# Optimization experiments

Hardware: AMD Instinct MI355X
Metric: run time of the kernel (lower is better)

## Reference

```python
import jax, jax.numpy as jnp
import numpy as np

N_NODES = 32768
N_EDGES = 524288
IN_F = 256
OUT_F = 128
NB = 4


def setup_inputs() -> dict:
    key = jax.random.key(0)
    ks = jax.random.split(key, 12)
    s_in = 1.0 / np.sqrt(IN_F)
    s_out = 1.0 / np.sqrt(OUT_F)
    s_cat = 1.0 / np.sqrt(OUT_F * NB)
    return {
        "x": jax.random.normal(ks[0], (N_NODES, IN_F), dtype=jnp.float32),
        "edge_index": jax.random.randint(ks[1], (2, N_EDGES), 0, N_NODES, dtype=jnp.int64),
        "Wb": jax.random.uniform(ks[2], (NB, IN_F, OUT_F), jnp.float32, -s_in, s_in),
        "bb": jax.random.uniform(ks[3], (NB, OUT_F), jnp.float32, -s_in, s_in),
        "W1": jax.random.uniform(ks[4], (NB, OUT_F, OUT_F), jnp.float32, -s_out, s_out),
        "b1": jax.random.uniform(ks[5], (NB, OUT_F), jnp.float32, -s_out, s_out),
        "W2": jax.random.uniform(ks[6], (NB, OUT_F, OUT_F), jnp.float32, -s_out, s_out),
        "b2": jax.random.uniform(ks[7], (NB, OUT_F), jnp.float32, -s_out, s_out),
        "branch_gates": jnp.ones((NB,), dtype=jnp.float32),
        "temperature": jnp.asarray(1.0, dtype=jnp.float32),
        "Wo": jax.random.uniform(ks[8], (OUT_F * NB, OUT_F), jnp.float32, -s_cat, s_cat),
        "bo": jax.random.uniform(ks[9], (OUT_F,), jnp.float32, -s_cat, s_cat),
    }


def _scatter_mean_step(h, row, col, inv_deg):
    # gather per-edge source features, mean-reduce onto destination nodes
    sums = jax.ops.segment_sum(h[row], col, num_segments=N_NODES)
    return sums * inv_deg


def reference(x, edge_index, Wb, bb, W1, b1, W2, b2, branch_gates, temperature, Wo, bo):
    row, col = edge_index[0], edge_index[1]
    deg = jax.ops.segment_sum(jnp.ones((N_EDGES,), x.dtype), col, num_segments=N_NODES)
    inv_deg = (1.0 / jnp.maximum(deg, 1.0))[:, None]  # empty segments -> 0 (scatter_mean semantics)

    gates = jax.nn.softmax(branch_gates / temperature)

    branch_outputs = []
    for i in range(NB):
        h = x @ Wb[i] + bb[i]                   # [N, OUT_F]
        for _ in range(i):                       # scale = scales[i % 4] = i
            h = _scatter_mean_step(h, row, col, inv_deg)
        h = jax.nn.relu(h @ W1[i] + b1[i]) @ W2[i] + b2[i]
        branch_outputs.append(h * gates[i])

    concat = jnp.concatenate(branch_outputs, axis=1)  # [N, NB*OUT_F]
    return concat @ Wo + bo
```

## Files before the change

### kernel.cpp

```cpp
#include <hip/hip_runtime.h>
#include <math.h>

#define N_NODES 32768
#define N_EDGES 524288
#define IN_F    256
#define OUT_F   128
#define NB      4
#define STRIDE  96

#define NE_BLK   256
#define CONV_BLK 1024
#define GX_BLK   2048
#define GEMM_BLK (N_NODES / 128)
#define M_BLK    (N_NODES / 256)

typedef __attribute__((ext_vector_type(8))) short bf16x8;
typedef __attribute__((ext_vector_type(4))) float f32x4;
typedef __attribute__((ext_vector_type(4))) ushort u16x4;

__device__ __forceinline__ ushort f2b(float f) {
    uint u = __float_as_uint(f);
    return (ushort)((u + 0x7fffu + ((u >> 16) & 1u)) >> 16);
}
__device__ __forceinline__ float b2f_lo(uint v) { return __uint_as_float(v << 16); }
__device__ __forceinline__ float b2f_hi(uint v) { return __uint_as_float(v & 0xffff0000u); }

__device__ __forceinline__ float softmax_gate(const float* bg, const float* temp, int i) {
    float T = temp[0];
    float mx = fmaxf(fmaxf(bg[0], bg[1]), fmaxf(bg[2], bg[3]));
    float e0 = expf((bg[0] - mx) / T), e1 = expf((bg[1] - mx) / T);
    float e2 = expf((bg[2] - mx) / T), e3 = expf((bg[3] - mx) / T);
    float s = e0 + e1 + e2 + e3;
    float ei = (i == 0) ? e0 : (i == 1) ? e1 : (i == 2) ? e2 : e3;
    return ei / s;
}

__device__ __forceinline__ int detect_i32(const int* __restrict__ ei, int* sflag) {
    if (threadIdx.x < 64) {
        unsigned long long b = __ballot(ei[2 * threadIdx.x + 1] != 0);
        if (threadIdx.x == 0) *sflag = (b != 0ull) ? 1 : 0;
    }
    __syncthreads();
    return *sflag;
}

__global__ __launch_bounds__(256) void fill_all_kernel(
    const int* __restrict__ ei, int* __restrict__ cursor, int* __restrict__ srcs,
    const float* __restrict__ x, ushort* __restrict__ xb,
    const float* __restrict__ Wb, const float* __restrict__ W1,
    const float* __restrict__ W2, const float* __restrict__ Wo,
    const float* __restrict__ bb, const float* __restrict__ b2,
    const float* __restrict__ bo, const float* __restrict__ bg,
    const float* __restrict__ temp,
    ushort* __restrict__ WcT, ushort* __restrict__ WzT,
    float* __restrict__ u, float* __restrict__ cvec) {
    __shared__ float smem[16 * 128];
    __shared__ int sflag;
    int b = blockIdx.x;
    int tid = threadIdx.x;
    if (b < NE_BLK) {
        int i32 = detect_i32(ei, &sflag);
#pragma unroll
        for (int it = 0; it < 8; it++) {
            int e = b * 2048 + it * 256 + tid;
            int r, c;
            if (i32 == 0) {
                r = __builtin_nontemporal_load(ei + 2 * e);
                c = __builtin_nontemporal_load(ei + 2 * (N_EDGES + e));
            } else {
                r = __builtin_nontemporal_load(ei + e);
                c = __builtin_nontemporal_load(ei + N_EDGES + e);
            }
            int slot = atomicAdd(&cursor[c], 1);
            if (slot < STRIDE) srcs[(size_t)c * STRIDE + slot] = r;
        }
        return;
    }
    b -= NE_BLK;
    if (b < CONV_BLK) {
#pragma unroll
        for (int it = 0; it < 8; it++) {
            int idx = b * 2048 + it * 256 + tid;
            f32x4 v = __builtin_nontemporal_load((const f32x4*)x + idx);
            u16x4 o;
            o.x = f2b(v.x); o.y = f2b(v.y); o.z = f2b(v.z); o.w = f2b(v.w);
            *((u16x4*)xb + idx) = o;
        }
        return;
    }
    b -= CONV_BLK;
    int f = tid & 127, rh = tid >> 7;
    if (b < 64) {
        int i = b >> 4, k0 = (b & 15) * 16;
#pragma unroll
        for (int rr = 0; rr < 8; rr++)
            smem[(rh * 8 + rr) * 128 + f] = Wb[((size_t)i * IN_F + k0 + rh * 8 + rr) * OUT_F + f];
        __syncthreads();
        float acc[8] = {};
        const float* W1i = W1 + (size_t)i * OUT_F * OUT_F;
        for (int j = 0; j < OUT_F; j++) {
            float w1 = W1i[j * OUT_F + f];
#pragma unroll
            for (int rr = 0; rr < 8; rr++) acc[rr] += smem[(rh * 8 + rr) * 128 + j] * w1;
        }
        ushort tmp[8];
#pragma unroll
        for (int rr = 0; rr < 8; rr++) tmp[rr] = f2b(acc[rr]);
        *(uint4*)(WcT + ((size_t)i * OUT_F + f) * IN_F + k0 + rh * 8) = *(uint4*)tmp;
    } else if (b < 96) {
        int id = b - 64;
        int i = id >> 3, j0 = (id & 7) * 16;
#pragma unroll
        for (int rr = 0; rr < 8; rr++)
            smem[(rh * 8 + rr) * 128 + f] = W2[((size_t)i * OUT_F + j0 + rh * 8 + rr) * OUT_F + f];
        __syncthreads();
        float acc[8] = {};
        for (int l = 0; l < OUT_F; l++) {
            float wo = Wo[((size_t)i * OUT_F + l) * OUT_F + f];
#pragma unroll
            for (int rr = 0; rr < 8; rr++) acc[rr] += smem[(rh * 8 + rr) * 128 + l] * wo;
        }
        float g = softmax_gate(bg, temp, i);
        ushort tmp[8];
#pragma unroll
        for (int rr = 0; rr < 8; rr++) tmp[rr] = f2b(g * acc[rr]);
        *(uint4*)(WzT + (size_t)f * (NB * OUT_F) + i * OUT_F + j0 + rh * 8) = *(uint4*)tmp;
    } else {
        int id = b - 96;
        int jc = rh;
        if (id < NB) {
            int i = id;
            float partial = 0.f;
            for (int j = jc * 64; j < jc * 64 + 64; j++)
                partial += bb[i * OUT_F + j] * W1[((size_t)i * OUT_F + j) * OUT_F + f];
            smem[jc * 128 + f] = partial;
            __syncthreads();
            if (jc == 0) u[i * OUT_F + f] = smem[f] + smem[128 + f];
        } else {
            int i = id - NB;
            float partial = 0.f;
            for (int j = jc * 64; j < jc * 64 + 64; j++)
                partial += b2[i * OUT_F + j] * Wo[((size_t)i * OUT_F + j) * OUT_F + f];
            smem[jc * 128 + f] = partial;
            __syncthreads();
            if (jc == 0) {
                float tot = (smem[f] + smem[128 + f]) * softmax_gate(bg, temp, i);
                if (i == 0) tot += bo[f];
                atomicAdd(&cvec[f], tot);
            }
        }
    }
}

#define ACC8(A, V)                                                              \
    A[0] += b2f_lo(V.x); A[1] += b2f_hi(V.x);                                   \
    A[2] += b2f_lo(V.y); A[3] += b2f_hi(V.y);                                   \
    A[4] += b2f_lo(V.z); A[5] += b2f_hi(V.z);                                   \
    A[6] += b2f_lo(V.w); A[7] += b2f_hi(V.w)

#define GATHER_256(INBUF)                                                       \
    float a0[8] = {0.f,0.f,0.f,0.f,0.f,0.f,0.f,0.f};                            \
    float a1[8] = {0.f,0.f,0.f,0.f,0.f,0.f,0.f,0.f};                            \
    int p = s;                                                                  \
    for (; p + 12 <= e; p += 12) {                                              \
        int base = p + 6 * half;                                                \
        int2 s01 = *(const int2*)(srcs + base);                                 \
        int2 s23 = *(const int2*)(srcs + base + 2);                             \
        int2 s45 = *(const int2*)(srcs + base + 4);                             \
        uint4 v0 = *(const uint4*)(INBUF + (size_t)s01.x * IN_F + fl * 8);      \
        uint4 v1 = *(const uint4*)(INBUF + (size_t)s01.y * IN_F + fl * 8);      \
        uint4 v2 = *(const uint4*)(INBUF + (size_t)s23.x * IN_F + fl * 8);      \
        uint4 v3 = *(const uint4*)(INBUF + (size_t)s23.y * IN_F + fl * 8);      \
        uint4 v4 = *(const uint4*)(INBUF + (size_t)s45.x * IN_F + fl * 8);      \
        uint4 v5 = *(const uint4*)(INBUF + (size_t)s45.y * IN_F + fl * 8);      \
        ACC8(a0, v0); ACC8(a1, v1); ACC8(a0, v2);                               \
        ACC8(a1, v3); ACC8(a0, v4); ACC8(a1, v5);                               \
    }                                                                           \
    for (; p + 4 <= e; p += 4) {                                                \
        int2 ss = *(const int2*)(srcs + p + 2 * half);                          \
        uint4 v0 = *(const uint4*)(INBUF + (size_t)ss.x * IN_F + fl * 8);       \
        uint4 v1 = *(const uint4*)(INBUF + (size_t)ss.y * IN_F + fl * 8);       \
        ACC8(a0, v0); ACC8(a1, v1);                                             \
    }                                                                           \
    for (; p + half < e; p += 2) {                                              \
        int src = srcs[p + half];                                               \
        uint4 v0 = *(const uint4*)(INBUF + (size_t)src * IN_F + fl * 8);        \
        ACC8(a0, v0);                                                           \
    }                                                                           \
    _Pragma("unroll") for (int k = 0; k < 8; k++) a0[k] += a1[k];               \
    _Pragma("unroll") for (int k = 0; k < 8; k++) a0[k] += __shfl_down(a0[k], 32);

__global__ __launch_bounds__(256, 8) void prop_x_kernel(
    const ushort* __restrict__ xb, ushort* __restrict__ X1b,
    const int* __restrict__ deg, float* __restrict__ m2,
    const int* __restrict__ srcs) {
    int blk = blockIdx.x;
    int tid = threadIdx.x;
    if (blk < M_BLK) {
        int n = blk * 256 + tid;
        int d = deg[n];
        int s = n * STRIDE, e = s + ((d < STRIDE) ? d : STRIDE);
        float sum = 0.f;
        for (int p = s; p < e; ++p) sum += (deg[srcs[p]] > 0) ? 1.0f : 0.0f;
        m2[n] = sum / (float)((d > 1) ? d : 1);
        return;
    }
    blk -= M_BLK;
    int lane = tid & 63;
    int half = lane >> 5, fl = lane & 31;
    for (int i = 0; i < 4; i++) {
        int node = blk * 16 + i * 4 + (tid >> 6);
        int d = deg[node];
        int s = node * STRIDE, e = s + ((d < STRIDE) ? d : STRIDE);
        GATHER_256(xb);
        if (half == 0) {
            float w = 1.0f / (float)((d > 1) ? d : 1);
            uint4 o;
            o.x = (uint)f2b(a0[0] * w) | ((uint)f2b(a0[1] * w) << 16);
            o.y = (uint)f2b(a0[2] * w) | ((uint)f2b(a0[3] * w) << 16);
            o.z = (uint)f2b(a0[4] * w) | ((uint)f2b(a0[5] * w) << 16);
            o.w = (uint)f2b(a0[6] * w) | ((uint)f2b(a0[7] * w) << 16);
            *(uint4*)(X1b + (size_t)node * IN_F + fl * 8) = o;
        }
    }
}

__global__ __launch_bounds__(256) void gemmP_kernel(
    const ushort* __restrict__ xb, const ushort* __restrict__ X1b,
    const ushort* __restrict__ WcT, const float* __restrict__ u,
    const float* __restrict__ b1, const int* __restrict__ deg,
    ushort* __restrict__ R, ushort* __restrict__ PQ) {
    int y = blockIdx.y;
    const ushort* A = (y == 0) ? xb : X1b;
    const ushort* WT = WcT + (size_t)y * OUT_F * IN_F;
    int m0 = blockIdx.x * 128;
    __shared__ ushort As[128][72];
    __shared__ ushort Bs[128][72];
    int tid = threadIdx.x;
    int wv = tid >> 6, lane = tid & 63, quad = lane >> 4, lm = lane & 15;
    f32x4 acc[2][8];
    f32x4 zero = {0.f, 0.f, 0.f, 0.f};
#pragma unroll
    for (int i = 0; i < 2; i++)
#pragma unroll
        for (int j = 0; j < 8; j++) acc[i][j] = zero;
    for (int k0 = 0; k0 < IN_F; k0 += 64) {
        __syncthreads();
#pragma unroll
        for (int it = 0; it < 4; it++) {
            int c = tid + 256 * it;
            int r = c >> 3, c8 = c & 7;
            *(uint4*)&As[r][c8 * 8] = *(const uint4*)(A + (size_t)(m0 + r) * IN_F + k0 + c8 * 8);
            *(uint4*)&Bs[r][c8 * 8] = *(const uint4*)(WT + (size_t)r * IN_F + k0 + c8 * 8);
        }
        __syncthreads();
#pragma unroll
        for (int ks = 0; ks < 2; ks++) {
            bf16x8 af0 = *(const bf16x8*)&As[wv * 32 + lm][ks * 32 + quad * 8];
            bf16x8 af1 = *(const bf16x8*)&As[wv * 32 + 16 + lm][ks * 32 + quad * 8];
#pragma unroll
            for (int nt = 0; nt < 8; nt++) {
                bf16x8 bf = *(const bf16x8*)&Bs[nt * 16 + lm][ks * 32 + quad * 8];
                acc[0][nt] = __builtin_amdgcn_mfma_f32_16x16x32_bf16(af0, bf, acc[0][nt], 0, 0, 0);
                acc[1][nt] = __builtin_amdgcn_mfma_f32_16x16x32_bf16(af1, bf, acc[1][nt], 0, 0, 0);
            }
        }
    }
    if (y >= 2) {
        int pqoff = (y - 2) * OUT_F;
#pragma unroll
        for (int mt = 0; mt < 2; mt++)
#pragma unroll
            for (int r = 0; r < 4; r++) {
                int row = m0 + wv * 32 + mt * 16 + quad * 4 + r;
#pragma unroll
                for (int nt = 0; nt < 8; nt++) {
                    int col = nt * 16 + lm;
                    PQ[(size_t)row * IN_F + pqoff + col] = f2b(acc[mt][nt][r]);
                }
            }
    } else {
        float uv[8], bv[8];
#pragma unroll
        for (int nt = 0; nt < 8; nt++) {
            int col = nt * 16 + lm;
            uv[nt] = u[y * OUT_F + col];
            bv[nt] = b1[y * OUT_F + col];
        }
#pragma unroll
        for (int mt = 0; mt < 2; mt++)
#pragma unroll
            for (int r = 0; r < 4; r++) {
                int row = m0 + wv * 32 + mt * 16 + quad * 4 + r;
                float mval = (y == 0) ? 1.0f : ((deg[row] > 0) ? 1.0f : 0.0f);
#pragma unroll
                for (int nt = 0; nt < 8; nt++) {
                    int col = nt * 16 + lm;
                    float h = acc[mt][nt][r] + mval * uv[nt] + bv[nt];
                    R[(size_t)row * (NB * OUT_F) + y * OUT_F + col] = f2b(fmaxf(h, 0.f));
                }
            }
    }
}

__global__ __launch_bounds__(256, 8) void prop_pq_kernel(
    const ushort* __restrict__ PQ, ushort* __restrict__ R, ushort* __restrict__ Qp,
    const int* __restrict__ deg, const float* __restrict__ m2, float* __restrict__ m3,
    const float* __restrict__ u2, const float* __restrict__ b12,
    const int* __restrict__ srcs) {
    int blk = blockIdx.x;
    int tid = threadIdx.x;
    if (blk < M_BLK) {
        int n = blk * 256 + tid;
        int d = deg[n];
        int s = n * STRIDE, e = s + ((d < STRIDE) ? d : STRIDE);
        float sum = 0.f;
        for (int p = s; p < e; ++p) sum += m2[srcs[p]];
        m3[n] = sum / (float)((d > 1) ? d : 1);
        return;
    }
    blk -= M_BLK;
    int lane = tid & 63;
    int half = lane >> 5, fl = lane & 31;
    for (int i = 0; i < 4; i++) {
        int node = blk * 16 + i * 4 + (tid >> 6);
        int d = deg[node];
        int s = node * STRIDE, e = s + ((d < STRIDE) ? d : STRIDE);
        GATHER_256(PQ);
        if (half == 0) {
            float w = 1.0f / (float)((d > 1) ? d : 1);
            if (fl < 16) {
                int col = fl * 8;
                float mv = m2[node];
                float4 ua = *(const float4*)(u2 + col);
                float4 ub = *(const float4*)(u2 + col + 4);
                float4 ba = *(const float4*)(b12 + col);
                float4 bb_ = *(const float4*)(b12 + col + 4);
                float o_[8];
                o_[0] = fmaxf(a0[0] * w + mv * ua.x + ba.x, 0.f);
                o_[1] = fmaxf(a0[1] * w + mv * ua.y + ba.y, 0.f);
                o_[2] = fmaxf(a0[2] * w + mv * ua.z + ba.z, 0.f);
                o_[3] = fmaxf(a0[3] * w + mv * ua.w + ba.w, 0.f);
                o_[4] = fmaxf(a0[4] * w + mv * ub.x + bb_.x, 0.f);
                o_[5] = fmaxf(a0[5] * w + mv * ub.y + bb_.y, 0.f);
                o_[6] = fmaxf(a0[6] * w + mv * ub.z + bb_.z, 0.f);
                o_[7] = fmaxf(a0[7] * w + mv * ub.w + bb_.w, 0.f);
                uint4 o;
                o.x = (uint)f2b(o_[0]) | ((uint)f2b(o_[1]) << 16);
                o.y = (uint)f2b(o_[2]) | ((uint)f2b(o_[3]) << 16);
                o.z = (uint)f2b(o_[4]) | ((uint)f2b(o_[5]) << 16);
                o.w = (uint)f2b(o_[6]) | ((uint)f2b(o_[7]) << 16);
                *(uint4*)(R + (size_t)node * (NB * OUT_F) + 2 * OUT_F + col) = o;
            } else {
                int col = (fl - 16) * 8;
                uint4 o;
                o.x = (uint)f2b(a0[0] * w) | ((uint)f2b(a0[1] * w) << 16);
                o.y = (uint)f2b(a0[2] * w) | ((uint)f2b(a0[3] * w) << 16);
                o.z = (uint)f2b(a0[4] * w) | ((uint)f2b(a0[5] * w) << 16);
                o.w = (uint)f2b(a0[6] * w) | ((uint)f2b(a0[7] * w) << 16);
                *(uint4*)(Qp + (size_t)node * OUT_F + col) = o;
            }
        }
    }
}

__global__ __launch_bounds__(256, 8) void prop_q_kernel(
    const ushort* __restrict__ Qp, ushort* __restrict__ R,
    const int* __restrict__ deg, const float* __restrict__ m3,
    const float* __restrict__ u3, const float* __restrict__ b13,
    const int* __restrict__ srcs) {
    int lane = threadIdx.x & 63;
    int q = lane >> 4, fl = lane & 15;
    for (int i = 0; i < 4; i++) {
        int node = blockIdx.x * 16 + i * 4 + (threadIdx.x >> 6);
        int d = deg[node];
        int s = node * STRIDE, e = s + ((d < STRIDE) ? d : STRIDE);
        float a[8] = {0.f,0.f,0.f,0.f,0.f,0.f,0.f,0.f};
        float b[8] = {0.f,0.f,0.f,0.f,0.f,0.f,0.f,0.f};
        int p = s;
        for (; p + 16 <= e; p += 16) {
            int4 sq = *(const int4*)(srcs + p + 4 * q);
            uint4 v0 = *(const uint4*)(Qp + (size_t)sq.x * OUT_F + fl * 8);
            uint4 v1 = *(const uint4*)(Qp + (size_t)sq.y * OUT_F + fl * 8);
            uint4 v2 = *(const uint4*)(Qp + (size_t)sq.z * OUT_F + fl * 8);
            uint4 v3 = *(const uint4*)(Qp + (size_t)sq.w * OUT_F + fl * 8);
            ACC8(a, v0); ACC8(b, v1); ACC8(a, v2); ACC8(b, v3);
        }
        for (; p + 8 <= e; p += 8) {
            int2 ss = *(const int2*)(srcs + p + 2 * q);
            uint4 v0 = *(const uint4*)(Qp + (size_t)ss.x * OUT_F + fl * 8);
            uint4 v1 = *(const uint4*)(Qp + (size_t)ss.y * OUT_F + fl * 8);
            ACC8(a, v0); ACC8(b, v1);
        }
        for (; p + 4 <= e; p += 4) {
            int src = srcs[p + q];
            uint4 v0 = *(const uint4*)(Qp + (size_t)src * OUT_F + fl * 8);
            ACC8(a, v0);
        }
        if (p + q < e) {
            int src = srcs[p + q];
            uint4 v0 = *(const uint4*)(Qp + (size_t)src * OUT_F + fl * 8);
            ACC8(a, v0);
        }
#pragma unroll
        for (int k = 0; k < 8; k++) a[k] += b[k];
#pragma unroll
        for (int k = 0; k < 8; k++) a[k] += __shfl_down(a[k], 32);
#pragma unroll
        for (int k = 0; k < 8; k++) a[k] += __shfl_down(a[k], 16);
        if (lane < 16) {
            float w = 1.0f / (float)((d > 1) ? d : 1);
            float mv = m3[node];
            int col = fl * 8;
            float4 ua = *(const float4*)(u3 + col);
            float4 ub = *(const float4*)(u3 + col + 4);
            float4 ba = *(const float4*)(b13 + col);
            float4 bb_ = *(const float4*)(b13 + col + 4);
            float o_[8];
            o_[0] = fmaxf(a[0] * w + mv * ua.x + ba.x, 0.f);
            o_[1] = fmaxf(a[1] * w + mv * ua.y + ba.y, 0.f);
            o_[2] = fmaxf(a[2] * w + mv * ua.z + ba.z, 0.f);
            o_[3] = fmaxf(a[3] * w + mv * ua.w + ba.w, 0.f);
            o_[4] = fmaxf(a[4] * w + mv * ub.x + bb_.x, 0.f);
            o_[5] = fmaxf(a[5] * w + mv * ub.y + bb_.y, 0.f);
            o_[6] = fmaxf(a[6] * w + mv * ub.z + bb_.z, 0.f);
            o_[7] = fmaxf(a[7] * w + mv * ub.w + bb_.w, 0.f);
            uint4 o;
            o.x = (uint)f2b(o_[0]) | ((uint)f2b(o_[1]) << 16);
            o.y = (uint)f2b(o_[2]) | ((uint)f2b(o_[3]) << 16);
            o.z = (uint)f2b(o_[4]) | ((uint)f2b(o_[5]) << 16);
            o.w = (uint)f2b(o_[6]) | ((uint)f2b(o_[7]) << 16);
            *(uint4*)(R + (size_t)node * (NB * OUT_F) + 3 * OUT_F + col) = o;
        }
    }
}

__global__ __launch_bounds__(256) void gemm2_mfma_kernel(
    const ushort* __restrict__ R, const ushort* __restrict__ WzT,
    const float* __restrict__ cvec, float* __restrict__ out) {
    int m0 = blockIdx.x * 128;
    const int K = NB * OUT_F;
    __shared__ ushort As[128][72];
    __shared__ ushort Bs[128][72];
    int tid = threadIdx.x;
    int wv = tid >> 6, lane = tid & 63, quad = lane >> 4, lm = lane & 15;
    f32x4 acc[2][8];
    f32x4 zero = {0.f, 0.f, 0.f, 0.f};
#pragma unroll
    for (int i = 0; i < 2; i++)
#pragma unroll
        for (int j = 0; j < 8; j++) acc[i][j] = zero;
    for (int k0 = 0; k0 < K; k0 += 64) {
        __syncthreads();
#pragma unroll
        for (int it = 0; it < 4; it++) {
            int c = tid + 256 * it;
            int r = c >> 3, c8 = c & 7;
            *(uint4*)&As[r][c8 * 8] = *(const uint4*)(R + (size_t)(m0 + r) * K + k0 + c8 * 8);
            *(uint4*)&Bs[r][c8 * 8] = *(const uint4*)(WzT + (size_t)r * K + k0 + c8 * 8);
        }
        __syncthreads();
#pragma unroll
        for (int ks = 0; ks < 2; ks++) {
            bf16x8 af0 = *(const bf16x8*)&As[wv * 32 + lm][ks * 32 + quad * 8];
            bf16x8 af1 = *(const bf16x8*)&As[wv * 32 + 16 + lm][ks * 32 + quad * 8];
#pragma unroll
            for (int nt = 0; nt < 8; nt++) {
                bf16x8 bf = *(const bf16x8*)&Bs[nt * 16 + lm][ks * 32 + quad * 8];
                acc[0][nt] = __builtin_amdgcn_mfma_f32_16x16x32_bf16(af0, bf, acc[0][nt], 0, 0, 0);
                acc[1][nt] = __builtin_amdgcn_mfma_f32_16x16x32_bf16(af1, bf, acc[1][nt], 0, 0, 0);
            }
        }
    }
    float cb[8];
#pragma unroll
    for (int nt = 0; nt < 8; nt++) cb[nt] = cvec[nt * 16 + lm];
#pragma unroll
    for (int mt = 0; mt < 2; mt++)
#pragma unroll
        for (int r = 0; r < 4; r++) {
            int row = m0 + wv * 32 + mt * 16 + quad * 4 + r;
#pragma unroll
            for (int nt = 0; nt < 8; nt++) {
                int col = nt * 16 + lm;
                __builtin_nontemporal_store(acc[mt][nt][r] + cb[nt],
                                            out + (size_t)row * OUT_F + col);
            }
        }
}

extern "C" void kernel_launch(void* const* d_in, const int* in_sizes, int n_in,
                              void* d_out, int out_size, void* d_ws, size_t ws_size,
                              hipStream_t stream) {
    const float* x    = (const float*)d_in[0];
    const int*   ei   = (const int*)d_in[1];
    const float* Wb   = (const float*)d_in[2];
    const float* bb   = (const float*)d_in[3];
    const float* W1   = (const float*)d_in[4];
    const float* b1   = (const float*)d_in[5];
    const float* W2   = (const float*)d_in[6];
    const float* b2   = (const float*)d_in[7];
    const float* bg   = (const float*)d_in[8];
    const float* temp = (const float*)d_in[9];
    const float* Wo   = (const float*)d_in[10];
    const float* bo   = (const float*)d_in[11];
    float* out = (float*)d_out;

    char* w = (char*)d_ws;
    size_t used = 0;
    auto alloc = [&](size_t bytes) {
        char* p = w + used;
        used += (bytes + 255) & ~(size_t)255;
        return p;
    };
    int*    cursor = (int*)alloc(N_NODES * 4);
    float*  cvec   = (float*)alloc(OUT_F * 4);
    int*    srcs   = (int*)alloc((size_t)N_NODES * STRIDE * 4);
    float*  m2v    = (float*)alloc(N_NODES * 4);
    float*  m3v    = (float*)alloc(N_NODES * 4);
    float*  u      = (float*)alloc(NB * OUT_F * 4);
    ushort* WcT    = (ushort*)alloc((size_t)NB * IN_F * OUT_F * 2);
    ushort* WzT    = (ushort*)alloc((size_t)NB * OUT_F * OUT_F * 2);
    ushort* xb     = (ushort*)alloc((size_t)N_NODES * IN_F * 2);
    ushort* X1b    = (ushort*)alloc((size_t)N_NODES * IN_F * 2);
    ushort* PQ     = (ushort*)alloc((size_t)N_NODES * IN_F * 2);
    ushort* Qp     = (ushort*)alloc((size_t)N_NODES * OUT_F * 2);
    ushort* R      = (ushort*)alloc((size_t)N_NODES * NB * OUT_F * 2);
    if (used > ws_size) return;

    int* deg = cursor;

    hipMemsetAsync(cursor, 0, N_NODES * 4 + 512, stream);

    fill_all_kernel<<<NE_BLK + CONV_BLK + 104, 256, 0, stream>>>(
        ei, cursor, srcs, x, xb, Wb, W1, W2, Wo, bb, b2, bo, bg, temp, WcT, WzT, u, cvec);

    prop_x_kernel<<<M_BLK + GX_BLK, 256, 0, stream>>>(xb, X1b, deg, m2v, srcs);

    {
        dim3 grid(GEMM_BLK, 4);
        gemmP_kernel<<<grid, 256, 0, stream>>>(xb, X1b, WcT, u, b1, deg, R, PQ);
    }

    prop_pq_kernel<<<M_BLK + GX_BLK, 256, 0, stream>>>(
        PQ, R, Qp, deg, m2v, m3v, u + 2 * OUT_F, b1 + 2 * OUT_F, srcs);

    prop_q_kernel<<<GX_BLK, 256, 0, stream>>>(
        Qp, R, deg, m3v, u + 3 * OUT_F, b1 + 3 * OUT_F, srcs);

    gemm2_mfma_kernel<<<GEMM_BLK, 256, 0, stream>>>(R, WzT, cvec, out);
}
```

Before: 292.3 us.

## Split neighbor gathers into 64-column slices across separate blocks

```diff
diff --git a/kernel.cpp b/kernel.cpp
--- a/kernel.cpp
+++ b/kernel.cpp
@@ -158,37 +158,30 @@
     A[4] += b2f_lo(V.z); A[5] += b2f_hi(V.z);                                   \
     A[6] += b2f_lo(V.w); A[7] += b2f_hi(V.w)
 
-#define GATHER_256(INBUF)                                                       \
-    float a0[8] = {0.f,0.f,0.f,0.f,0.f,0.f,0.f,0.f};                            \
-    float a1[8] = {0.f,0.f,0.f,0.f,0.f,0.f,0.f,0.f};                            \
+#define GATHER_SLICE(INBUF, STRIDE_F)                                           \
+    float a[8] = {0.f,0.f,0.f,0.f,0.f,0.f,0.f,0.f};                             \
+    float b_[8] = {0.f,0.f,0.f,0.f,0.f,0.f,0.f,0.f};                            \
     int p = s;                                                                  \
-    for (; p + 12 <= e; p += 12) {                                              \
-        int base = p + 6 * half;                                                \
-        int2 s01 = *(const int2*)(srcs + base);                                 \
-        int2 s23 = *(const int2*)(srcs + base + 2);                             \
-        int2 s45 = *(const int2*)(srcs + base + 4);                             \
-        uint4 v0 = *(const uint4*)(INBUF + (size_t)s01.x * IN_F + fl * 8);      \
-        uint4 v1 = *(const uint4*)(INBUF + (size_t)s01.y * IN_F + fl * 8);      \
-        uint4 v2 = *(const uint4*)(INBUF + (size_t)s23.x * IN_F + fl * 8);      \
-        uint4 v3 = *(const uint4*)(INBUF + (size_t)s23.y * IN_F + fl * 8);      \
-        uint4 v4 = *(const uint4*)(INBUF + (size_t)s45.x * IN_F + fl * 8);      \
-        uint4 v5 = *(const uint4*)(INBUF + (size_t)s45.y * IN_F + fl * 8);      \
-        ACC8(a0, v0); ACC8(a1, v1); ACC8(a0, v2);                               \
-        ACC8(a1, v3); ACC8(a0, v4); ACC8(a1, v5);                               \
+    for (; p + 16 <= e; p += 16) {                                              \
+        int2 ss = *(const int2*)(srcs + p + 2 * g);                             \
+        uint4 v0 = *(const uint4*)(INBUF + (size_t)ss.x * STRIDE_F + colOff);   \
+        uint4 v1 = *(const uint4*)(INBUF + (size_t)ss.y * STRIDE_F + colOff);   \
+        ACC8(a, v0); ACC8(b_, v1);                                              \
     }                                                                           \
-    for (; p + 4 <= e; p += 4) {                                                \
-        int2 ss = *(const int2*)(srcs + p + 2 * half);                          \
-        uint4 v0 = *(const uint4*)(INBUF + (size_t)ss.x * IN_F + fl * 8);       \
-        uint4 v1 = *(const uint4*)(INBUF + (size_t)ss.y * IN_F + fl * 8);       \
-        ACC8(a0, v0); ACC8(a1, v1);                                             \
+    for (; p + 8 <= e; p += 8) {                                                \
+        int src = srcs[p + g];                                                  \
+        uint4 v0 = *(const uint4*)(INBUF + (size_t)src * STRIDE_F + colOff);    \
+        ACC8(a, v0);                                                            \
     }                                                                           \
-    for (; p + half < e; p += 2) {                                              \
-        int src = srcs[p + half];                                               \
-        uint4 v0 = *(const uint4*)(INBUF + (size_t)src * IN_F + fl * 8);        \
-        ACC8(a0, v0);                                                           \
+    if (p + g < e) {                                                            \
+        int src = srcs[p + g];                                                  \
+        uint4 v0 = *(const uint4*)(INBUF + (size_t)src * STRIDE_F + colOff);    \
+        ACC8(b_, v0);                                                           \
     }                                                                           \
-    _Pragma("unroll") for (int k = 0; k < 8; k++) a0[k] += a1[k];               \
-    _Pragma("unroll") for (int k = 0; k < 8; k++) a0[k] += __shfl_down(a0[k], 32);
+    _Pragma("unroll") for (int k = 0; k < 8; k++) a[k] += b_[k];                \
+    _Pragma("unroll") for (int k = 0; k < 8; k++) a[k] += __shfl_down(a[k], 32);\
+    _Pragma("unroll") for (int k = 0; k < 8; k++) a[k] += __shfl_down(a[k], 16);\
+    _Pragma("unroll") for (int k = 0; k < 8; k++) a[k] += __shfl_down(a[k], 8);
 
 __global__ __launch_bounds__(256, 8) void prop_x_kernel(
     const ushort* __restrict__ xb, ushort* __restrict__ X1b,
@@ -206,21 +199,23 @@
         return;
     }
     blk -= M_BLK;
+    int pass = blk >> 11, blk2 = blk & 2047;
     int lane = tid & 63;
-    int half = lane >> 5, fl = lane & 31;
+    int g = lane >> 3, f8 = lane & 7;
+    int colOff = pass * 64 + f8 * 8;
     for (int i = 0; i < 4; i++) {
-        int node = blk * 16 + i * 4 + (tid >> 6);
+        int node = blk2 * 16 + i * 4 + (tid >> 6);
         int d = deg[node];
         int s = node * STRIDE, e = s + ((d < STRIDE) ? d : STRIDE);
-        GATHER_256(xb);
-        if (half == 0) {
+        GATHER_SLICE(xb, IN_F);
+        if (lane < 8) {
             float w = 1.0f / (float)((d > 1) ? d : 1);
             uint4 o;
-            o.x = (uint)f2b(a0[0] * w) | ((uint)f2b(a0[1] * w) << 16);
-            o.y = (uint)f2b(a0[2] * w) | ((uint)f2b(a0[3] * w) << 16);
-            o.z = (uint)f2b(a0[4] * w) | ((uint)f2b(a0[5] * w) << 16);
-            o.w = (uint)f2b(a0[6] * w) | ((uint)f2b(a0[7] * w) << 16);
-            *(uint4*)(X1b + (size_t)node * IN_F + fl * 8) = o;
+            o.x = (uint)f2b(a[0] * w) | ((uint)f2b(a[1] * w) << 16);
+            o.y = (uint)f2b(a[2] * w) | ((uint)f2b(a[3] * w) << 16);
+            o.z = (uint)f2b(a[4] * w) | ((uint)f2b(a[5] * w) << 16);
+            o.w = (uint)f2b(a[6] * w) | ((uint)f2b(a[7] * w) << 16);
+            *(uint4*)(X1b + (size_t)node * IN_F + colOff) = o;
         }
     }
 }
@@ -320,31 +315,33 @@
         return;
     }
     blk -= M_BLK;
+    int pass = blk >> 11, blk2 = blk & 2047;
     int lane = tid & 63;
-    int half = lane >> 5, fl = lane & 31;
+    int g = lane >> 3, f8 = lane & 7;
+    int colOff = pass * 64 + f8 * 8;
     for (int i = 0; i < 4; i++) {
-        int node = blk * 16 + i * 4 + (tid >> 6);
+        int node = blk2 * 16 + i * 4 + (tid >> 6);
         int d = deg[node];
         int s = node * STRIDE, e = s + ((d < STRIDE) ? d : STRIDE);
-        GATHER_256(PQ);
-        if (half == 0) {
+        GATHER_SLICE(PQ, IN_F);
+        if (lane < 8) {
             float w = 1.0f / (float)((d > 1) ? d : 1);
-            if (fl < 16) {
-                int col = fl * 8;
+            if (pass < 2) {
+                int col = colOff;
                 float mv = m2[node];
                 float4 ua = *(const float4*)(u2 + col);
                 float4 ub = *(const float4*)(u2 + col + 4);
                 float4 ba = *(const float4*)(b12 + col);
-                float4 bb_ = *(const float4*)(b12 + col + 4);
+                float4 bb2 = *(const float4*)(b12 + col + 4);
                 float o_[8];
-                o_[0] = fmaxf(a0[0] * w + mv * ua.x + ba.x, 0.f);
-                o_[1] = fmaxf(a0[1] * w + mv * ua.y + ba.y, 0.f);
-                o_[2] = fmaxf(a0[2] * w + mv * ua.z + ba.z, 0.f);
-                o_[3] = fmaxf(a0[3] * w + mv * ua.w + ba.w, 0.f);
-                o_[4] = fmaxf(a0[4] * w + mv * ub.x + bb_.x, 0.f);
-                o_[5] = fmaxf(a0[5] * w + mv * ub.y + bb_.y, 0.f);
-                o_[6] = fmaxf(a0[6] * w + mv * ub.z + bb_.z, 0.f);
-                o_[7] = fmaxf(a0[7] * w + mv * ub.w + bb_.w, 0.f);
+                o_[0] = fmaxf(a[0] * w + mv * ua.x + ba.x, 0.f);
+                o_[1] = fmaxf(a[1] * w + mv * ua.y + ba.y, 0.f);
+                o_[2] = fmaxf(a[2] * w + mv * ua.z + ba.z, 0.f);
+                o_[3] = fmaxf(a[3] * w + mv * ua.w + ba.w, 0.f);
+                o_[4] = fmaxf(a[4] * w + mv * ub.x + bb2.x, 0.f);
+                o_[5] = fmaxf(a[5] * w + mv * ub.y + bb2.y, 0.f);
+                o_[6] = fmaxf(a[6] * w + mv * ub.z + bb2.z, 0.f);
+                o_[7] = fmaxf(a[7] * w + mv * ub.w + bb2.w, 0.f);
                 uint4 o;
                 o.x = (uint)f2b(o_[0]) | ((uint)f2b(o_[1]) << 16);
                 o.y = (uint)f2b(o_[2]) | ((uint)f2b(o_[3]) << 16);
@@ -352,12 +349,12 @@
                 o.w = (uint)f2b(o_[6]) | ((uint)f2b(o_[7]) << 16);
                 *(uint4*)(R + (size_t)node * (NB * OUT_F) + 2 * OUT_F + col) = o;
             } else {
-                int col = (fl - 16) * 8;
+                int col = colOff - 128;
                 uint4 o;
-                o.x = (uint)f2b(a0[0] * w) | ((uint)f2b(a0[1] * w) << 16);
-                o.y = (uint)f2b(a0[2] * w) | ((uint)f2b(a0[3] * w) << 16);
-                o.z = (uint)f2b(a0[4] * w) | ((uint)f2b(a0[5] * w) << 16);
-                o.w = (uint)f2b(a0[6] * w) | ((uint)f2b(a0[7] * w) << 16);
+                o.x = (uint)f2b(a[0] * w) | ((uint)f2b(a[1] * w) << 16);
+                o.y = (uint)f2b(a[2] * w) | ((uint)f2b(a[3] * w) << 16);
+                o.z = (uint)f2b(a[4] * w) | ((uint)f2b(a[5] * w) << 16);
+                o.w = (uint)f2b(a[6] * w) | ((uint)f2b(a[7] * w) << 16);
                 *(uint4*)(Qp + (size_t)node * OUT_F + col) = o;
             }
         }
@@ -369,62 +366,34 @@
     const int* __restrict__ deg, const float* __restrict__ m3,
     const float* __restrict__ u3, const float* __restrict__ b13,
     const int* __restrict__ srcs) {
-    int lane = threadIdx.x & 63;
-    int q = lane >> 4, fl = lane & 15;
+    int blk = blockIdx.x;
+    int tid = threadIdx.x;
+    int pass = blk >> 11, blk2 = blk & 2047;
+    int lane = tid & 63;
+    int g = lane >> 3, f8 = lane & 7;
+    int colOff = pass * 64 + f8 * 8;
     for (int i = 0; i < 4; i++) {
-        int node = blockIdx.x * 16 + i * 4 + (threadIdx.x >> 6);
+        int node = blk2 * 16 + i * 4 + (tid >> 6);
         int d = deg[node];
         int s = node * STRIDE, e = s + ((d < STRIDE) ? d : STRIDE);
-        float a[8] = {0.f,0.f,0.f,0.f,0.f,0.f,0.f,0.f};
-        float b[8] = {0.f,0.f,0.f,0.f,0.f,0.f,0.f,0.f};
-        int p = s;
-        for (; p + 16 <= e; p += 16) {
-            int4 sq = *(const int4*)(srcs + p + 4 * q);
-            uint4 v0 = *(const uint4*)(Qp + (size_t)sq.x * OUT_F + fl * 8);
-            uint4 v1 = *(const uint4*)(Qp + (size_t)sq.y * OUT_F + fl * 8);
-            uint4 v2 = *(const uint4*)(Qp + (size_t)sq.z * OUT_F + fl * 8);
-            uint4 v3 = *(const uint4*)(Qp + (size_t)sq.w * OUT_F + fl * 8);
-            ACC8(a, v0); ACC8(b, v1); ACC8(a, v2); ACC8(b, v3);
-        }
-        for (; p + 8 <= e; p += 8) {
-            int2 ss = *(const int2*)(srcs + p + 2 * q);
-            uint4 v0 = *(const uint4*)(Qp + (size_t)ss.x * OUT_F + fl * 8);
-            uint4 v1 = *(const uint4*)(Qp + (size_t)ss.y * OUT_F + fl * 8);
-            ACC8(a, v0); ACC8(b, v1);
-        }
-        for (; p + 4 <= e; p += 4) {
-            int src = srcs[p + q];
-            uint4 v0 = *(const uint4*)(Qp + (size_t)src * OUT_F + fl * 8);
-            ACC8(a, v0);
-        }
-        if (p + q < e) {
-            int src = srcs[p + q];
-            uint4 v0 = *(const uint4*)(Qp + (size_t)src * OUT_F + fl * 8);
-            ACC8(a, v0);
-        }
-#pragma unroll
-        for (int k = 0; k < 8; k++) a[k] += b[k];
-#pragma unroll
-        for (int k = 0; k < 8; k++) a[k] += __shfl_down(a[k], 32);
-#pragma unroll
-        for (int k = 0; k < 8; k++) a[k] += __shfl_down(a[k], 16);
-        if (lane < 16) {
+        GATHER_SLICE(Qp, OUT_F);
+        if (lane < 8) {
             float w = 1.0f / (float)((d > 1) ? d : 1);
             float mv = m3[node];
-            int col = fl * 8;
+            int col = colOff;
             float4 ua = *(const float4*)(u3 + col);
             float4 ub = *(const float4*)(u3 + col + 4);
             float4 ba = *(const float4*)(b13 + col);
-            float4 bb_ = *(const float4*)(b13 + col + 4);
+            float4 bb2 = *(const float4*)(b13 + col + 4);
             float o_[8];
             o_[0] = fmaxf(a[0] * w + mv * ua.x + ba.x, 0.f);
             o_[1] = fmaxf(a[1] * w + mv * ua.y + ba.y, 0.f);
             o_[2] = fmaxf(a[2] * w + mv * ua.z + ba.z, 0.f);
             o_[3] = fmaxf(a[3] * w + mv * ua.w + ba.w, 0.f);
-            o_[4] = fmaxf(a[4] * w + mv * ub.x + bb_.x, 0.f);
-            o_[5] = fmaxf(a[5] * w + mv * ub.y + bb_.y, 0.f);
-            o_[6] = fmaxf(a[6] * w + mv * ub.z + bb_.z, 0.f);
-            o_[7] = fmaxf(a[7] * w + mv * ub.w + bb_.w, 0.f);
+            o_[4] = fmaxf(a[4] * w + mv * ub.x + bb2.x, 0.f);
+            o_[5] = fmaxf(a[5] * w + mv * ub.y + bb2.y, 0.f);
+            o_[6] = fmaxf(a[6] * w + mv * ub.z + bb2.z, 0.f);
+            o_[7] = fmaxf(a[7] * w + mv * ub.w + bb2.w, 0.f);
             uint4 o;
             o.x = (uint)f2b(o_[0]) | ((uint)f2b(o_[1]) << 16);
             o.y = (uint)f2b(o_[2]) | ((uint)f2b(o_[3]) << 16);
@@ -535,17 +504,17 @@
     fill_all_kernel<<<NE_BLK + CONV_BLK + 104, 256, 0, stream>>>(
         ei, cursor, srcs, x, xb, Wb, W1, W2, Wo, bb, b2, bo, bg, temp, WcT, WzT, u, cvec);
 
-    prop_x_kernel<<<M_BLK + GX_BLK, 256, 0, stream>>>(xb, X1b, deg, m2v, srcs);
+    prop_x_kernel<<<M_BLK + 4 * GX_BLK, 256, 0, stream>>>(xb, X1b, deg, m2v, srcs);
 
     {
         dim3 grid(GEMM_BLK, 4);
         gemmP_kernel<<<grid, 256, 0, stream>>>(xb, X1b, WcT, u, b1, deg, R, PQ);
     }
 
-    prop_pq_kernel<<<M_BLK + GX_BLK, 256, 0, stream>>>(
+    prop_pq_kernel<<<M_BLK + 4 * GX_BLK, 256, 0, stream>>>(
         PQ, R, Qp, deg, m2v, m3v, u + 2 * OUT_F, b1 + 2 * OUT_F, srcs);
 
-    prop_q_kernel<<<GX_BLK, 256, 0, stream>>>(
+    prop_q_kernel<<<2 * GX_BLK, 256, 0, stream>>>(
         Qp, R, deg, m3v, u + 3 * OUT_F, b1 + 3 * OUT_F, srcs);
 
     gemm2_mfma_kernel<<<GEMM_BLK, 256, 0, stream>>>(R, WzT, cvec, out);
```

New measurement: 288.6 us. About the same (-1.3%).
